# Kernel tuning notes

Measured on AMD Instinct MI355X. Metric: run time of the kernel, lower is better.

The kernel has to match this reference:

```python
import jax, jax.numpy as jnp
import numpy as np

B, NQ, NK, H = 4, 2048, 2048, 512
TEMP = 1.0


def setup_inputs() -> dict:
    key = jax.random.key(0)
    ks = jax.random.split(key, 13)
    s = 0.02
    inp = {
        "query_feat": jax.random.normal(ks[0], (B, NQ, H), jnp.float32),
        "key_feat": jax.random.normal(ks[1], (B, NK, H), jnp.float32),
        "qm_uncert": jax.random.normal(ks[2], (B, NQ), jnp.float32),
        "md_uncert": jax.random.normal(ks[3], (B, NK), jnp.float32),
        "Wq": jax.random.normal(ks[4], (H, H), jnp.float32) * s,
        "bq": jnp.zeros((H,), jnp.float32),
        "Wk": jax.random.normal(ks[5], (H, H), jnp.float32) * s,
        "bk": jnp.zeros((H,), jnp.float32),
        "Wv": jax.random.normal(ks[6], (H, H), jnp.float32) * s,
        "bv": jnp.zeros((H,), jnp.float32),
        "Wo": jax.random.normal(ks[7], (H, H), jnp.float32) * s,
        "bo": jnp.zeros((H,), jnp.float32),
        "tau": jnp.float32(1.0),
    }
    return inp


def reference(query_feat, key_feat, qm_uncert, md_uncert,
              Wq, bq, Wk, bk, Wv, bv, Wo, bo, tau):
    h = query_feat.shape[-1]
    Q = query_feat @ Wq.T + bq          # [B,Nq,H]
    K = key_feat @ Wk.T + bk            # [B,Nk,H]
    V = key_feat @ Wv.T + bv            # [B,Nk,H]

    # scaled dot-product logits
    logits = jnp.einsum('bqh,bkh->bqk', Q, K) / jnp.sqrt(jnp.asarray(h, logits_dtype(Q)))

    # uncertainty weight: sigmoid(tau * (qm_i + md_j)), then sanitize (mult mode)
    u = jax.nn.sigmoid(tau * (qm_uncert[:, :, None] + md_uncert[:, None, :]))
    u = jnp.nan_to_num(u, nan=1.0, posinf=1e6, neginf=1e-6)
    u = jnp.clip(u, 1e-6, 1e6)
    row_sum = jnp.sum(jnp.abs(u), axis=-1, keepdims=True)
    u = jnp.where(row_sum <= 1e-12, jnp.asarray(1e-6, u.dtype), u)

    logits = (logits * u) / TEMP

    # rows fully masked to -1e9 get zeroed (no mask here, but kept for faithfulness)
    all_masked = jnp.all(logits == -1e9, axis=-1, keepdims=True)
    logits = jnp.where(all_masked, jnp.zeros_like(logits), logits)

    attn = jax.nn.softmax(logits, axis=-1)  # dropout p=0 -> identity
    att = jnp.einsum('bqk,bkh->bqh', attn, V)
    out = att @ Wo.T + bo
    return out, attn


def logits_dtype(x):
    return x.dtype
```

## Files before the change

### kernel.cpp

```cpp
#include <hip/hip_runtime.h>
#include <stdint.h>

#define DEVI static __device__ __forceinline__

typedef unsigned short u16;
typedef short bf16x8 __attribute__((ext_vector_type(8)));
typedef u16 u16x8 __attribute__((ext_vector_type(8)));
typedef u16 u16x4 __attribute__((ext_vector_type(4)));
typedef float f32x4 __attribute__((ext_vector_type(4)));

DEVI u16 f2bf(float f) {
    uint32_t u = __builtin_bit_cast(uint32_t, f);
    u += 0x7FFFu + ((u >> 16) & 1u);
    return (u16)(u >> 16);
}
DEVI float bf2f(u16 u) { return __builtin_bit_cast(float, (uint32_t)u << 16); }

struct GemmArgs {
    const void* A;
    const void* A2;
    long long aStrideBytes;
    int lda;
    const u16* Bm;
    long long bStrideElts;
    int ldb;
    int K;
    const float* bias; const float* bias2; const float* bias3;
    u16* outB;
    float* outF;
    long long outFStride;
    const float* qm; const float* md; const float* tauPtr; float scale;
    float* partials;
    const float* invsPtr;
    float* invsOut;
    u16* vt;
};

enum { EPI_PROJ3 = 0, EPI_LOGITS = 1, EPI_LOGITSB = 2, EPI_PV = 3, EPI_OUT = 4 };

template <int EPI, int AMODE, int TM, bool U2>
__global__ __launch_bounds__(256, 4) void gemm_bt(GemmArgs p) {
    constexpr int NB = U2 ? 2 : 1;
    constexpr int NF = (TM == 128) ? 4 : 2;
    __shared__ u16 As[NB][TM * 32];
    __shared__ u16 Bs[NB][128 * 32];
    __shared__ float redBuf[2][128];
    __shared__ float sInvLds[128];

    const int tid = threadIdx.x;
    const int lane = tid & 63;
    const int wave = tid >> 6;
    const int g = lane >> 4, lr = lane & 15;
    const int waveRowBase = (TM == 128) ? (wave >> 1) * 64 : 0;
    const int waveColBase = (TM == 128) ? (wave & 1) * 64 : wave * 32;
    const int z = blockIdx.z;
    const int rowBase = blockIdx.x * TM;
    const int colBase = blockIdx.y * 128;

    int batch = z, koff = 0;
    if constexpr (EPI == EPI_PV) { batch = z & 3; koff = (z >> 2) * p.K; }

    const char* Abase;
    const float* bias = p.bias;
    const u16* Bbase;
    if constexpr (EPI == EPI_PROJ3) {
        Abase = (const char*)(z == 0 ? p.A : p.A2);
        Bbase = p.Bm + (size_t)z * 512 * 512;
        bias = (z == 0) ? p.bias : (z == 1 ? p.bias2 : p.bias3);
    } else {
        Abase = (const char*)p.A + (size_t)batch * p.aStrideBytes + (size_t)koff * (AMODE == 1 ? 4 : 2);
        Bbase = p.Bm + (size_t)batch * p.bStrideElts + koff;
    }

    if constexpr (EPI == EPI_PV && AMODE == 0) {
        if (blockIdx.y == 4) {
            if (tid < 128) {
                const float* pp = p.partials + ((size_t)batch * 2048 + rowBase + tid) * 16;
                float s = 0.f;
                #pragma unroll
                for (int t = 0; t < 16; ++t) s += pp[t];
                float inv = 1.0f / s;
                sInvLds[tid] = inv;
                p.invsOut[batch * 2048 + rowBase + tid] = inv;
            }
            __syncthreads();
            const u16* e = (const u16*)Abase + (size_t)rowBase * 2048;
            float* attnOut = p.outF + (size_t)batch * p.outFStride + (size_t)rowBase * 2048 + koff;
            #pragma unroll 4
            for (int it = 0; it < 64; ++it) {
                int cc = it * 256 + tid;
                int row = cc >> 7, colc = (cc & 127) * 8;
                float s = sInvLds[row];
                u16x8 v = *(const u16x8*)(e + (size_t)row * 2048 + colc);
                f32x4 f0, f1;
                f0[0] = bf2f(v[0]) * s; f0[1] = bf2f(v[1]) * s;
                f0[2] = bf2f(v[2]) * s; f0[3] = bf2f(v[3]) * s;
                f1[0] = bf2f(v[4]) * s; f1[1] = bf2f(v[5]) * s;
                f1[2] = bf2f(v[6]) * s; f1[3] = bf2f(v[7]) * s;
                float* dst = attnOut + (size_t)row * 2048 + colc;
                __builtin_nontemporal_store(f0, (f32x4*)dst);
                __builtin_nontemporal_store(f1, (f32x4*)dst + 1);
            }
            return;
        }
    }

    f32x4 acc[4][NF] = {};

    const int arow2 = tid >> 2, kh2 = (tid & 3) << 3;
    const u16* pa0 = nullptr; const u16* pa1 = nullptr; float sInv = 1.0f;
    if constexpr (AMODE == 2) {
        pa0 = (const u16*)p.A + (size_t)(rowBase + arow2) * 512 + kh2;
        pa1 = pa0 + (size_t)8192 * 512;
        sInv = p.invsPtr ? p.invsPtr[rowBase + arow2] : 1.0f;
    }

    const int nk = p.K >> 5;
    for (int kt = 0; kt < nk; kt += NB) {
        const int kb = kt << 5;
        float4 areg[4]; u16x8 a0, a1;
        if constexpr (AMODE == 1) {
            const float* Af = (const float*)Abase;
            const int arow = tid >> 1, kh = (tid & 1) << 4;
            const float* src = Af + (size_t)(rowBase + arow) * p.lda + kb + kh;
            #pragma unroll
            for (int j = 0; j < 4; ++j) areg[j] = ((const float4*)src)[j];
        } else if constexpr (AMODE == 2) {
            a0 = *(const u16x8*)(pa0 + kb);
            a1 = *(const u16x8*)(pa1 + kb);
        }
        __syncthreads();
        if constexpr (AMODE == 1) {
            const int arow = tid >> 1, kh = (tid & 1) << 4;
            u16 tmp[16];
            #pragma unroll
            for (int j = 0; j < 4; ++j) {
                tmp[4 * j + 0] = f2bf(areg[j].x);
                tmp[4 * j + 1] = f2bf(areg[j].y);
                tmp[4 * j + 2] = f2bf(areg[j].z);
                tmp[4 * j + 3] = f2bf(areg[j].w);
            }
            #pragma unroll
            for (int h = 0; h < 2; ++h)
                *(u16x8*)&As[0][arow * 32 + kh + h * 8] = *(u16x8*)&tmp[h * 8];
        } else if constexpr (AMODE == 2) {
            u16 tmp[8];
            #pragma unroll
            for (int j = 0; j < 8; ++j)
                tmp[j] = f2bf((bf2f(a0[j]) + bf2f(a1[j])) * sInv);
            *(u16x8*)&As[0][arow2 * 32 + kh2] = *(u16x8*)tmp;
        } else {
            #pragma unroll
            for (int b = 0; b < NB; ++b)
                #pragma unroll
                for (int i = 0; i < TM / 64; ++i) {
                    int c = i * 256 + tid;
                    const u16* gp = (const u16*)Abase + (size_t)(rowBase + (c >> 2)) * p.lda + kb + b * 32 + (c & 3) * 8;
                    char* lp = (char*)&As[b][0] + (i * 256 + wave * 64) * 16;
                    __builtin_amdgcn_global_load_lds((const __attribute__((address_space(1))) void*)gp,
                                                     (__attribute__((address_space(3))) void*)lp, 16, 0, 0);
                }
        }
        #pragma unroll
        for (int b = 0; b < NB; ++b)
            #pragma unroll
            for (int i = 0; i < 2; ++i) {
                int c = i * 256 + tid;
                const u16* gp = Bbase + (size_t)(colBase + (c >> 2)) * p.ldb + kb + b * 32 + (c & 3) * 8;
                char* lp = (char*)&Bs[b][0] + (i * 256 + wave * 64) * 16;
                __builtin_amdgcn_global_load_lds((const __attribute__((address_space(1))) void*)gp,
                                                 (__attribute__((address_space(3))) void*)lp, 16, 0, 0);
            }
        __syncthreads();

        #pragma unroll
        for (int b = 0; b < NB; ++b) {
            bf16x8 af[4], bfr[NF];
            #pragma unroll
            for (int m = 0; m < 4; ++m)
                af[m] = *(const bf16x8*)&As[b][(waveRowBase + m * 16 + lr) * 32 + g * 8];
            #pragma unroll
            for (int n = 0; n < NF; ++n)
                bfr[n] = *(const bf16x8*)&Bs[b][(waveColBase + n * 16 + lr) * 32 + g * 8];
            #pragma unroll
            for (int m = 0; m < 4; ++m)
                #pragma unroll
                for (int n = 0; n < NF; ++n)
                    acc[m][n] = __builtin_amdgcn_mfma_f32_16x16x32_bf16(af[m], bfr[n], acc[m][n], 0, 0, 0);
        }
    }

    const int rB = rowBase + waveRowBase;
    const int cB = colBase + waveColBase;

    if constexpr (EPI == EPI_PROJ3) {
        if (z < 2) {
            u16* dst = p.outB + (size_t)z * 8192 * 512;
            #pragma unroll
            for (int n = 0; n < NF; ++n) {
                int col = cB + n * 16 + lr;
                float bv = bias[col];
                #pragma unroll
                for (int m = 0; m < 4; ++m) {
                    int r0 = rB + m * 16 + g * 4;
                    #pragma unroll
                    for (int i = 0; i < 4; ++i)
                        dst[(size_t)(r0 + i) * 512 + col] = f2bf(acc[m][n][i] + bv);
                }
            }
        } else {
            #pragma unroll
            for (int n = 0; n < NF; ++n) {
                int col = cB + n * 16 + lr;
                float bv = bias[col];
                #pragma unroll
                for (int m = 0; m < 4; ++m) {
                    int r0 = rB + m * 16 + g * 4;
                    int b = r0 >> 11, k0 = r0 & 2047;
                    u16x4 pk;
                    #pragma unroll
                    for (int i = 0; i < 4; ++i) pk[i] = f2bf(acc[m][n][i] + bv);
                    *(u16x4*)&p.vt[((size_t)b * 512 + col) * 2048 + k0] = pk;
                }
            }
        }
    } else if constexpr (EPI == EPI_LOGITS || EPI == EPI_LOGITSB) {
        const float* qmB = p.qm + z * 2048;
        const float* mdB = p.md + z * 2048;
        const float tau = *p.tauPtr;
        float* outRow = p.outF + (size_t)z * p.outFStride;
        float mdv[NF];
        #pragma unroll
        for (int n = 0; n < NF; ++n) mdv[n] = mdB[cB + n * 16 + lr];
        #pragma unroll
        for (int m = 0; m < 4; ++m) {
            int r0 = rB + m * 16 + g * 4;
            #pragma unroll
            for (int i = 0; i < 4; ++i) {
                int q = r0 + i;
                float qv = qmB[q];
                float rs = 0.f;
                #pragma unroll
                for (int n = 0; n < NF; ++n) {
                    float t = tau * (qv + mdv[n]);
                    float u = 1.0f / (1.0f + __expf(-t));
                    u = fminf(fmaxf(u, 1e-6f), 1e6f);
                    float e = __expf(acc[m][n][i] * p.scale * u);
                    if (EPI == EPI_LOGITSB)
                        p.outB[((size_t)(z * 2048 + q)) * 2048 + cB + n * 16 + lr] = f2bf(e);
                    else
                        outRow[(size_t)q * 2048 + cB + n * 16 + lr] = e;
                    rs += e;
                }
                #pragma unroll
                for (int off = 1; off < 16; off <<= 1) rs += __shfl_xor(rs, off, 64);
                if (lr == 0) redBuf[wave & 1][waveRowBase + m * 16 + g * 4 + i] = rs;
            }
        }
        __syncthreads();
        if (tid < 128) {
            float s = redBuf[0][tid] + redBuf[1][tid];
            int q = rowBase + tid;
            p.partials[((size_t)z * 2048 + q) * 16 + blockIdx.y] = s;
        }
    } else if constexpr (EPI == EPI_PV) {
        const int split = z >> 2;
        u16* dst = p.outB + (size_t)split * 8192 * 512;
        #pragma unroll
        for (int n = 0; n < NF; ++n) {
            int col = cB + n * 16 + lr;
            #pragma unroll
            for (int m = 0; m < 4; ++m) {
                int r0 = rB + m * 16 + g * 4;
                size_t gr = (size_t)batch * 2048 + r0;
                #pragma unroll
                for (int i = 0; i < 4; ++i)
                    dst[(gr + i) * 512 + col] = f2bf(acc[m][n][i]);
            }
        }
    } else {
        #pragma unroll
        for (int n = 0; n < NF; ++n) {
            int col = cB + n * 16 + lr;
            float bv = p.bias[col];
            #pragma unroll
            for (int m = 0; m < 4; ++m) {
                int r0 = rB + m * 16 + g * 4;
                #pragma unroll
                for (int i = 0; i < 4; ++i)
                    __builtin_nontemporal_store(acc[m][n][i] + bv, &p.outF[(size_t)(r0 + i) * 512 + col]);
            }
        }
    }
}

__global__ void cvt_all(const float* Wq, const float* Wk, const float* Wv, const float* Wo,
                        const float* qf, const float* kf,
                        u16* wdst, u16* qdst, u16* kdst) {
    const size_t WSZ = (size_t)512 * 512;
    const size_t FSZ = (size_t)8192 * 512;
    size_t i = ((size_t)blockIdx.x * 256 + threadIdx.x) * 4;
    const float* src; u16* dst; size_t off;
    if (i < 4 * WSZ) {
        int w = (int)(i / WSZ);
        src = w == 0 ? Wq : w == 1 ? Wk : w == 2 ? Wv : Wo;
        off = i - (size_t)w * WSZ;
        dst = wdst + i;
    } else if (i < 4 * WSZ + FSZ) {
        src = qf; off = i - 4 * WSZ; dst = qdst + off;
    } else {
        src = kf; off = i - 4 * WSZ - FSZ; dst = kdst + off;
    }
    float4 v = *(const float4*)(src + off);
    u16x4 u = { f2bf(v.x), f2bf(v.y), f2bf(v.z), f2bf(v.w) };
    *(u16x4*)(dst + off - (off - (dst == wdst + i ? 0 : 0))) = u;
}

__global__ void cvt_all2(const float* Wq, const float* Wk, const float* Wv, const float* Wo,
                         const float* qf, const float* kf,
                         u16* wdst, u16* qdst, u16* kdst) {
    const size_t WSZ = (size_t)512 * 512;
    const size_t FSZ = (size_t)8192 * 512;
    size_t i = ((size_t)blockIdx.x * 256 + threadIdx.x) * 4;
    const float* src; u16* dstp;
    if (i < 4 * WSZ) {
        int w = (int)(i / WSZ);
        src = (w == 0 ? Wq : w == 1 ? Wk : w == 2 ? Wv : Wo) + (i - (size_t)w * WSZ);
        dstp = wdst + i;
    } else if (i < 4 * WSZ + FSZ) {
        size_t off = i - 4 * WSZ;
        src = qf + off; dstp = qdst + off;
    } else {
        size_t off = i - 4 * WSZ - FSZ;
        src = kf + off; dstp = kdst + off;
    }
    float4 v = *(const float4*)src;
    u16x4 u = { f2bf(v.x), f2bf(v.y), f2bf(v.z), f2bf(v.w) };
    *(u16x4*)dstp = u;
}

__global__ void rowsum_inv(const float* __restrict__ partials, float* __restrict__ invs) {
    int r = blockIdx.x * 256 + threadIdx.x;
    float s = 0.f;
    #pragma unroll
    for (int t = 0; t < 16; ++t) s += partials[r * 16 + t];
    invs[r] = 1.0f / s;
}

__global__ void normalize_attn(float* __restrict__ attn, const float* __restrict__ invs) {
    size_t i4 = (size_t)blockIdx.x * 256 + threadIdx.x;
    int row = (int)(i4 >> 9);
    float s = invs[row];
    float4 v = ((const float4*)attn)[i4];
    v.x *= s; v.y *= s; v.z *= s; v.w *= s;
    ((float4*)attn)[i4] = v;
}

extern "C" void kernel_launch(void* const* d_in, const int* in_sizes, int n_in,
                              void* d_out, int out_size, void* d_ws, size_t ws_size,
                              hipStream_t stream) {
    const float* qf  = (const float*)d_in[0];
    const float* kf  = (const float*)d_in[1];
    const float* qm  = (const float*)d_in[2];
    const float* md  = (const float*)d_in[3];
    const float* Wq  = (const float*)d_in[4];
    const float* bq  = (const float*)d_in[5];
    const float* Wk  = (const float*)d_in[6];
    const float* bk  = (const float*)d_in[7];
    const float* Wv  = (const float*)d_in[8];
    const float* bv  = (const float*)d_in[9];
    const float* Wo  = (const float*)d_in[10];
    const float* bo  = (const float*)d_in[11];
    const float* tau = (const float*)d_in[12];

    float* out  = (float*)d_out;
    float* attn = out + (size_t)4 * 2048 * 512;

    const size_t NV = (size_t)8192 * 512;
    u16* Qb   = (u16*)d_ws;
    u16* Kb   = Qb + NV;
    u16* Vtb  = Kb + NV;
    u16* Wqb  = Vtb + NV;
    u16* Wob  = Wqb + (size_t)3 * 512 * 512;
    float* partials = (float*)(Wqb + (size_t)4 * 512 * 512);
    float* invs = partials + (size_t)8192 * 16;
    u16* attE = (u16*)(invs + 8192);
    u16* qfB  = attE + (size_t)4 * 2048 * 2048;
    u16* kfB  = qfB + NV;
    size_t need = (size_t)((char*)(kfB + NV) - (char*)d_ws);
    const bool big = ws_size >= need;

    u16* partialPV = Qb;

    dim3 blk(256);

    GemmArgs a = {};
    a.lda = 512; a.ldb = 512; a.K = 512;
    a.bias = bq; a.bias2 = bk; a.bias3 = bv;
    a.outB = Qb; a.vt = Vtb;
    if (big) {
        cvt_all2<<<dim3(9216), blk, 0, stream>>>(Wq, Wk, Wv, Wo, qf, kf, Wqb, qfB, kfB);
        a.A = qfB; a.A2 = kfB; a.Bm = Wqb;
        gemm_bt<EPI_PROJ3, 0, 128, true><<<dim3(64, 4, 3), blk, 0, stream>>>(a);
    } else {
        cvt_all2<<<dim3(1024), blk, 0, stream>>>(Wq, Wk, Wv, Wo, qf, kf, Wqb, nullptr, nullptr);
        a.A = qf; a.A2 = kf; a.Bm = Wqb;
        gemm_bt<EPI_PROJ3, 1, 128, false><<<dim3(64, 4, 3), blk, 0, stream>>>(a);
    }

    GemmArgs lg = {};
    lg.A = Qb; lg.aStrideBytes = (long long)2048 * 512 * 2; lg.lda = 512;
    lg.Bm = Kb; lg.bStrideElts = (long long)2048 * 512; lg.ldb = 512;
    lg.K = 512;
    lg.qm = qm; lg.md = md; lg.tauPtr = tau;
    lg.scale = 0.04419417382415922f;
    lg.partials = partials;
    if (big) {
        lg.outB = attE;
        gemm_bt<EPI_LOGITSB, 0, 128, true><<<dim3(16, 16, 4), blk, 0, stream>>>(lg);
    } else {
        lg.outF = attn; lg.outFStride = (long long)2048 * 2048;
        gemm_bt<EPI_LOGITS, 0, 128, true><<<dim3(16, 16, 4), blk, 0, stream>>>(lg);
    }

    GemmArgs pv = {};
    pv.Bm = Vtb; pv.bStrideElts = (long long)512 * 2048; pv.ldb = 2048;
    pv.K = 1024; pv.outB = partialPV; pv.lda = 2048;
    pv.partials = partials; pv.invsOut = invs;
    if (big) {
        pv.A = attE; pv.aStrideBytes = (long long)2048 * 2048 * 2;
        pv.outF = attn; pv.outFStride = (long long)2048 * 2048;
        gemm_bt<EPI_PV, 0, 128, true><<<dim3(16, 5, 8), blk, 0, stream>>>(pv);
    } else {
        rowsum_inv<<<dim3(32), blk, 0, stream>>>(partials, invs);
        normalize_attn<<<dim3(16384), blk, 0, stream>>>(attn, invs);
        pv.A = attn; pv.aStrideBytes = (long long)2048 * 2048 * 4;
        gemm_bt<EPI_PV, 1, 128, false><<<dim3(16, 4, 8), blk, 0, stream>>>(pv);
    }

    GemmArgs og = {};
    og.A = partialPV; og.lda = 512;
    og.Bm = Wob; og.ldb = 512;
    og.K = 512; og.bias = bo; og.outF = out;
    og.invsPtr = big ? invs : nullptr;
    gemm_bt<EPI_OUT, 2, 64, false><<<dim3(128, 4, 1), blk, 0, stream>>>(og);
}
```

Measured before the change: 126.0 us.

## Double-buffer LDS loads in bf16 GEMM mainloop to overlap fetch with MFMA

Replaces the two-K-tiles-per-sync (U2) scheme in the AMODE 0 GEMM path with a ping-pong LDS pipeline. The next K tile is issued by async global_load_lds into the alternate buffer while MFMAs run on the current one, with one wait and barrier per iteration. It also raises wave priority around the MFMA block with s_setprio. The non-bf16 A paths now always allocate double LDS buffers, which may reduce occupancy for those variants, and an unused conversion kernel is removed.

```diff
diff --git a/kernel.cpp b/kernel.cpp
--- a/kernel.cpp
+++ b/kernel.cpp
@@ -38,12 +38,11 @@
 
 enum { EPI_PROJ3 = 0, EPI_LOGITS = 1, EPI_LOGITSB = 2, EPI_PV = 3, EPI_OUT = 4 };
 
-template <int EPI, int AMODE, int TM, bool U2>
+template <int EPI, int AMODE, int TM>
 __global__ __launch_bounds__(256, 4) void gemm_bt(GemmArgs p) {
-    constexpr int NB = U2 ? 2 : 1;
     constexpr int NF = (TM == 128) ? 4 : 2;
-    __shared__ u16 As[NB][TM * 32];
-    __shared__ u16 Bs[NB][128 * 32];
+    __shared__ u16 As[2][TM * 32];
+    __shared__ u16 Bs[2][128 * 32];
     __shared__ float redBuf[2][128];
     __shared__ float sInvLds[128];
 
@@ -107,81 +106,110 @@
 
     f32x4 acc[4][NF] = {};
 
-    const int arow2 = tid >> 2, kh2 = (tid & 3) << 3;
-    const u16* pa0 = nullptr; const u16* pa1 = nullptr; float sInv = 1.0f;
-    if constexpr (AMODE == 2) {
-        pa0 = (const u16*)p.A + (size_t)(rowBase + arow2) * 512 + kh2;
-        pa1 = pa0 + (size_t)8192 * 512;
-        sInv = p.invsPtr ? p.invsPtr[rowBase + arow2] : 1.0f;
-    }
-
     const int nk = p.K >> 5;
-    for (int kt = 0; kt < nk; kt += NB) {
-        const int kb = kt << 5;
-        float4 areg[4]; u16x8 a0, a1;
-        if constexpr (AMODE == 1) {
-            const float* Af = (const float*)Abase;
-            const int arow = tid >> 1, kh = (tid & 1) << 4;
-            const float* src = Af + (size_t)(rowBase + arow) * p.lda + kb + kh;
-            #pragma unroll
-            for (int j = 0; j < 4; ++j) areg[j] = ((const float4*)src)[j];
-        } else if constexpr (AMODE == 2) {
-            a0 = *(const u16x8*)(pa0 + kb);
-            a1 = *(const u16x8*)(pa1 + kb);
-        }
-        __syncthreads();
-        if constexpr (AMODE == 1) {
-            const int arow = tid >> 1, kh = (tid & 1) << 4;
-            u16 tmp[16];
-            #pragma unroll
-            for (int j = 0; j < 4; ++j) {
-                tmp[4 * j + 0] = f2bf(areg[j].x);
-                tmp[4 * j + 1] = f2bf(areg[j].y);
-                tmp[4 * j + 2] = f2bf(areg[j].z);
-                tmp[4 * j + 3] = f2bf(areg[j].w);
-            }
-            #pragma unroll
-            for (int h = 0; h < 2; ++h)
-                *(u16x8*)&As[0][arow * 32 + kh + h * 8] = *(u16x8*)&tmp[h * 8];
-        } else if constexpr (AMODE == 2) {
-            u16 tmp[8];
-            #pragma unroll
-            for (int j = 0; j < 8; ++j)
-                tmp[j] = f2bf((bf2f(a0[j]) + bf2f(a1[j])) * sInv);
-            *(u16x8*)&As[0][arow2 * 32 + kh2] = *(u16x8*)tmp;
-        } else {
-            #pragma unroll
-            for (int b = 0; b < NB; ++b)
-                #pragma unroll
-                for (int i = 0; i < TM / 64; ++i) {
-                    int c = i * 256 + tid;
-                    const u16* gp = (const u16*)Abase + (size_t)(rowBase + (c >> 2)) * p.lda + kb + b * 32 + (c & 3) * 8;
-                    char* lp = (char*)&As[b][0] + (i * 256 + wave * 64) * 16;
-                    __builtin_amdgcn_global_load_lds((const __attribute__((address_space(1))) void*)gp,
-                                                     (__attribute__((address_space(3))) void*)lp, 16, 0, 0);
-                }
-        }
-        #pragma unroll
-        for (int b = 0; b < NB; ++b)
+
+    if constexpr (AMODE == 0) {
+        auto stage = [&](int buf, int kt) {
+            const int kb = kt << 5;
+            #pragma unroll
+            for (int i = 0; i < TM / 64; ++i) {
+                int c = i * 256 + tid;
+                const u16* gp = (const u16*)Abase + (size_t)(rowBase + (c >> 2)) * p.lda + kb + (c & 3) * 8;
+                char* lp = (char*)&As[buf][0] + (i * 256 + wave * 64) * 16;
+                __builtin_amdgcn_global_load_lds((const __attribute__((address_space(1))) void*)gp,
+                                                 (__attribute__((address_space(3))) void*)lp, 16, 0, 0);
+            }
             #pragma unroll
             for (int i = 0; i < 2; ++i) {
                 int c = i * 256 + tid;
-                const u16* gp = Bbase + (size_t)(colBase + (c >> 2)) * p.ldb + kb + b * 32 + (c & 3) * 8;
-                char* lp = (char*)&Bs[b][0] + (i * 256 + wave * 64) * 16;
+                const u16* gp = Bbase + (size_t)(colBase + (c >> 2)) * p.ldb + kb + (c & 3) * 8;
+                char* lp = (char*)&Bs[buf][0] + (i * 256 + wave * 64) * 16;
                 __builtin_amdgcn_global_load_lds((const __attribute__((address_space(1))) void*)gp,
                                                  (__attribute__((address_space(3))) void*)lp, 16, 0, 0);
             }
-        __syncthreads();
-
-        #pragma unroll
-        for (int b = 0; b < NB; ++b) {
+        };
+        stage(0, 0);
+        asm volatile("s_waitcnt vmcnt(0)" ::: "memory");
+        __builtin_amdgcn_s_barrier();
+        for (int kt = 0; kt < nk; ++kt) {
+            const int cur = kt & 1;
+            if (kt + 1 < nk) stage(cur ^ 1, kt + 1);
             bf16x8 af[4], bfr[NF];
             #pragma unroll
             for (int m = 0; m < 4; ++m)
-                af[m] = *(const bf16x8*)&As[b][(waveRowBase + m * 16 + lr) * 32 + g * 8];
+                af[m] = *(const bf16x8*)&As[cur][(waveRowBase + m * 16 + lr) * 32 + g * 8];
             #pragma unroll
             for (int n = 0; n < NF; ++n)
-                bfr[n] = *(const bf16x8*)&Bs[b][(waveColBase + n * 16 + lr) * 32 + g * 8];
+                bfr[n] = *(const bf16x8*)&Bs[cur][(waveColBase + n * 16 + lr) * 32 + g * 8];
+            __builtin_amdgcn_s_setprio(1);
+            #pragma unroll
+            for (int m = 0; m < 4; ++m)
+                #pragma unroll
+                for (int n = 0; n < NF; ++n)
+                    acc[m][n] = __builtin_amdgcn_mfma_f32_16x16x32_bf16(af[m], bfr[n], acc[m][n], 0, 0, 0);
+            __builtin_amdgcn_s_setprio(0);
+            asm volatile("s_waitcnt vmcnt(0)" ::: "memory");
+            __builtin_amdgcn_s_barrier();
+        }
+    } else {
+        const int arow2 = tid >> 2, kh2 = (tid & 3) << 3;
+        const u16* pa0 = nullptr; const u16* pa1 = nullptr; float sInv = 1.0f;
+        if constexpr (AMODE == 2) {
+            pa0 = (const u16*)p.A + (size_t)(rowBase + arow2) * 512 + kh2;
+            pa1 = pa0 + (size_t)8192 * 512;
+            sInv = p.invsPtr ? p.invsPtr[rowBase + arow2] : 1.0f;
+        }
+        for (int kt = 0; kt < nk; ++kt) {
+            const int kb = kt << 5;
+            float4 areg[4]; u16x8 a0, a1;
+            if constexpr (AMODE == 1) {
+                const float* Af = (const float*)Abase;
+                const int arow = tid >> 1, kh = (tid & 1) << 4;
+                const float* src = Af + (size_t)(rowBase + arow) * p.lda + kb + kh;
+                #pragma unroll
+                for (int j = 0; j < 4; ++j) areg[j] = ((const float4*)src)[j];
+            } else {
+                a0 = *(const u16x8*)(pa0 + kb);
+                a1 = *(const u16x8*)(pa1 + kb);
+            }
+            __syncthreads();
+            if constexpr (AMODE == 1) {
+                const int arow = tid >> 1, kh = (tid & 1) << 4;
+                u16 tmp[16];
+                #pragma unroll
+                for (int j = 0; j < 4; ++j) {
+                    tmp[4 * j + 0] = f2bf(areg[j].x);
+                    tmp[4 * j + 1] = f2bf(areg[j].y);
+                    tmp[4 * j + 2] = f2bf(areg[j].z);
+                    tmp[4 * j + 3] = f2bf(areg[j].w);
+                }
+                #pragma unroll
+                for (int h = 0; h < 2; ++h)
+                    *(u16x8*)&As[0][arow * 32 + kh + h * 8] = *(u16x8*)&tmp[h * 8];
+            } else {
+                u16 tmp[8];
+                #pragma unroll
+                for (int j = 0; j < 8; ++j)
+                    tmp[j] = f2bf((bf2f(a0[j]) + bf2f(a1[j])) * sInv);
+                *(u16x8*)&As[0][arow2 * 32 + kh2] = *(u16x8*)tmp;
+            }
+            #pragma unroll
+            for (int i = 0; i < 2; ++i) {
+                int c = i * 256 + tid;
+                const u16* gp = Bbase + (size_t)(colBase + (c >> 2)) * p.ldb + kb + (c & 3) * 8;
+                char* lp = (char*)&Bs[0][0] + (i * 256 + wave * 64) * 16;
+                __builtin_amdgcn_global_load_lds((const __attribute__((address_space(1))) void*)gp,
+                                                 (__attribute__((address_space(3))) void*)lp, 16, 0, 0);
+            }
+            __syncthreads();
+
+            bf16x8 af[4], bfr[NF];
+            #pragma unroll
+            for (int m = 0; m < 4; ++m)
+                af[m] = *(const bf16x8*)&As[0][(waveRowBase + m * 16 + lr) * 32 + g * 8];
+            #pragma unroll
+            for (int n = 0; n < NF; ++n)
+                bfr[n] = *(const bf16x8*)&Bs[0][(waveColBase + n * 16 + lr) * 32 + g * 8];
             #pragma unroll
             for (int m = 0; m < 4; ++m)
                 #pragma unroll
@@ -292,28 +320,6 @@
             }
         }
     }
-}
-
-__global__ void cvt_all(const float* Wq, const float* Wk, const float* Wv, const float* Wo,
-                        const float* qf, const float* kf,
-                        u16* wdst, u16* qdst, u16* kdst) {
-    const size_t WSZ = (size_t)512 * 512;
-    const size_t FSZ = (size_t)8192 * 512;
-    size_t i = ((size_t)blockIdx.x * 256 + threadIdx.x) * 4;
-    const float* src; u16* dst; size_t off;
-    if (i < 4 * WSZ) {
-        int w = (int)(i / WSZ);
-        src = w == 0 ? Wq : w == 1 ? Wk : w == 2 ? Wv : Wo;
-        off = i - (size_t)w * WSZ;
-        dst = wdst + i;
-    } else if (i < 4 * WSZ + FSZ) {
-        src = qf; off = i - 4 * WSZ; dst = qdst + off;
-    } else {
-        src = kf; off = i - 4 * WSZ - FSZ; dst = kdst + off;
-    }
-    float4 v = *(const float4*)(src + off);
-    u16x4 u = { f2bf(v.x), f2bf(v.y), f2bf(v.z), f2bf(v.w) };
-    *(u16x4*)(dst + off - (off - (dst == wdst + i ? 0 : 0))) = u;
 }
 
 __global__ void cvt_all2(const float* Wq, const float* Wk, const float* Wv, const float* Wo,
@@ -401,11 +407,11 @@
     if (big) {
         cvt_all2<<<dim3(9216), blk, 0, stream>>>(Wq, Wk, Wv, Wo, qf, kf, Wqb, qfB, kfB);
         a.A = qfB; a.A2 = kfB; a.Bm = Wqb;
-        gemm_bt<EPI_PROJ3, 0, 128, true><<<dim3(64, 4, 3), blk, 0, stream>>>(a);
+        gemm_bt<EPI_PROJ3, 0, 128><<<dim3(64, 4, 3), blk, 0, stream>>>(a);
     } else {
         cvt_all2<<<dim3(1024), blk, 0, stream>>>(Wq, Wk, Wv, Wo, qf, kf, Wqb, nullptr, nullptr);
         a.A = qf; a.A2 = kf; a.Bm = Wqb;
-        gemm_bt<EPI_PROJ3, 1, 128, false><<<dim3(64, 4, 3), blk, 0, stream>>>(a);
+        gemm_bt<EPI_PROJ3, 1, 128><<<dim3(64, 4, 3), blk, 0, stream>>>(a);
     }
 
     GemmArgs lg = {};
@@ -417,10 +423,10 @@
     lg.partials = partials;
     if (big) {
         lg.outB = attE;
-        gemm_bt<EPI_LOGITSB, 0, 128, true><<<dim3(16, 16, 4), blk, 0, stream>>>(lg);
+        gemm_bt<EPI_LOGITSB, 0, 128><<<dim3(16, 16, 4), blk, 0, stream>>>(lg);
     } else {
         lg.outF = attn; lg.outFStride = (long long)2048 * 2048;
-        gemm_bt<EPI_LOGITS, 0, 128, true><<<dim3(16, 16, 4), blk, 0, stream>>>(lg);
+        gemm_bt<EPI_LOGITS, 0, 128><<<dim3(16, 16, 4), blk, 0, stream>>>(lg);
     }
 
     GemmArgs pv = {};
@@ -430,12 +436,12 @@
     if (big) {
         pv.A = attE; pv.aStrideBytes = (long long)2048 * 2048 * 2;
         pv.outF = attn; pv.outFStride = (long long)2048 * 2048;
-        gemm_bt<EPI_PV, 0, 128, true><<<dim3(16, 5, 8), blk, 0, stream>>>(pv);
+        gemm_bt<EPI_PV, 0, 128><<<dim3(16, 5, 8), blk, 0, stream>>>(pv);
     } else {
         rowsum_inv<<<dim3(32), blk, 0, stream>>>(partials, invs);
         normalize_attn<<<dim3(16384), blk, 0, stream>>>(attn, invs);
         pv.A = attn; pv.aStrideBytes = (long long)2048 * 2048 * 4;
-        gemm_bt<EPI_PV, 1, 128, false><<<dim3(16, 4, 8), blk, 0, stream>>>(pv);
+        gemm_bt<EPI_PV, 1, 128><<<dim3(16, 4, 8), blk, 0, stream>>>(pv);
     }
 
     GemmArgs og = {};
@@ -443,5 +449,5 @@
     og.Bm = Wob; og.ldb = 512;
     og.K = 512; og.bias = bo; og.outF = out;
     og.invsPtr = big ? invs : nullptr;
-    gemm_bt<EPI_OUT, 2, 64, false><<<dim3(128, 4, 1), blk, 0, stream>>>(og);
-}
+    gemm_bt<EPI_OUT, 2, 64><<<dim3(128, 4, 1), blk, 0, stream>>>(og);
+}
```

Result: no change. 128.2 us (+1.7%).
